# Optimization experiments

Hardware: AMD Instinct MI355X
Metric: run time of the kernel (lower is better)

The kernel has to match this reference:

```python
import jax, jax.numpy as jnp
import numpy as np

N = 50000          # number of nodes
A = 32             # anchor_set_num
D = 64             # latdim


def setup_inputs() -> dict:
    key = jax.random.key(0)
    k1, k2, k3, k4, k5 = jax.random.split(key, 5)
    embeds = jax.random.normal(k1, (N, D), dtype=jnp.float32)
    dists_array = jax.random.uniform(k2, (A, N), dtype=jnp.float32)
    anchor_set_id = jax.random.randint(k3, (A,), 0, N)
    # nn.Linear(2*latdim, latdim): weight [D, 2D], bias [D]
    bound = 1.0 / np.sqrt(2 * D)
    W_hidden = jax.random.uniform(k4, (D, 2 * D), minval=-bound, maxval=bound, dtype=jnp.float32)
    b_hidden = jax.random.uniform(k5, (D,), minval=-bound, maxval=bound, dtype=jnp.float32)
    return {"embeds": embeds, "dists_array": dists_array,
            "anchor_set_id": anchor_set_id,
            "W_hidden": W_hidden, "b_hidden": b_hidden}


def reference(embeds, dists_array, anchor_set_id, W_hidden, b_hidden):
    n, d = embeds.shape
    a = anchor_set_id.shape[0]
    # set_ids_emb.repeat(N,1).reshape(N, A, D) reduces to broadcasting anchors over nodes
    set_ids_emb = embeds[anchor_set_id]                       # [A, D]
    # messages[n, a] = set_ids_emb[a] * dists[a, n]
    messages = set_ids_emb[None, :, :] * dists_array.T[:, :, None]   # [N, A, D]
    # embeds.repeat(A,1).reshape(N, A, D): element [i, j] = embeds[(i*A + j) % N]
    self_feature = jnp.tile(embeds, (a, 1)).reshape(n, a, d)         # [N, A, D]
    # concat + Linear(2D -> D) expressed as split matmul (same math, no concat buffer)
    W1 = W_hidden[:, :d]   # acts on messages
    W2 = W_hidden[:, d:]   # acts on self_feature
    hidden = (jnp.einsum('nad,kd->nak', messages, W1)
              + jnp.einsum('nad,kd->nak', self_feature, W2)
              + b_hidden)                                            # [N, A, D]
    return jnp.mean(hidden, axis=1)                                  # [N, D]
```

## Files before the change

kernel.cpp:

```cpp
#include <hip/hip_runtime.h>


constexpr int N_PTS  = 50000;
constexpr int A_ANCH = 32;
constexpr int D_DIM  = 64;
constexpr int NSB    = 3125;
constexpr int TN     = 16;
constexpr int TILES  = N_PTS / TN;
constexpr int XSTR   = 36;
constexpr int PREP_TILE   = 16;
constexpr int PREP_BLOCKS = (NSB + PREP_TILE - 1) / PREP_TILE;

__global__ __launch_bounds__(256) void prep_kernel(
        const float* __restrict__ embeds,
        const int*   __restrict__ aid,
        const float* __restrict__ W,
        float*       __restrict__ M1,
        float*       __restrict__ SBW)
{
    const int t = threadIdx.x;

    if (blockIdx.x == PREP_BLOCKS) {
        for (int idx = t; idx < A_ANCH * D_DIM; idx += 256) {
            int a = idx >> 6, k = idx & 63;
            const float* erow = embeds + (size_t)aid[a] * D_DIM;
            const float* wrow = W + (size_t)k * 128;
            float s = 0.0f;
#pragma unroll
            for (int d = 0; d < D_DIM; ++d) s += erow[d] * wrow[d];
            M1[idx] = s * (1.0f / 32.0f);
        }
        return;
    }

    __shared__ float w2[64 * 64];
    __shared__ float sb[PREP_TILE * 64];

    {
        int k  = t & 63;
        int d0 = (t >> 6) * 16;
        const float* wr = W + (size_t)k * 128 + 64;
#pragma unroll
        for (int q = 0; q < 16; ++q) w2[(d0 + q) * 64 + k] = wr[d0 + q];
    }

    const int i0 = blockIdx.x * PREP_TILE;
    {
        int d = t & 63, il0 = t >> 6;
        for (int il = il0; il < PREP_TILE; il += 4) {
            int i = i0 + il;
            if (i >= NSB) break;
            int base = 16 * i;
            float s = 0.0f;
#pragma unroll
            for (int j = 0; j < 32; ++j) {
                int r = base + j;
                if (r >= N_PTS) r -= N_PTS;
                s += embeds[(size_t)r * D_DIM + d];
            }
            sb[il * 64 + d] = s;
        }
    }
    __syncthreads();
    {
        int k = t & 63, il0 = t >> 6;
        for (int il = il0; il < PREP_TILE; il += 4) {
            int i = i0 + il;
            if (i >= NSB) break;
            const float* srow = sb + il * 64;
            float s = 0.0f;
#pragma unroll
            for (int d = 0; d < D_DIM; ++d) s += srow[d] * w2[d * 64 + k];
            SBW[(size_t)i * 64 + k] = s * (1.0f / 32.0f);
        }
    }
}

__global__ __launch_bounds__(256, 4) void pnn_main(
        const float* __restrict__ dists,
        const float* __restrict__ b,
        const float* __restrict__ M1,
        const float* __restrict__ SBW,
        float*       __restrict__ out)
{
    __shared__ float m1s[A_ANCH * D_DIM];
    __shared__ float xs[TN * XSTR];

    const int t = threadIdx.x;

    {
        const float4* M4 = (const float4*)M1;
        float4*       s4 = (float4*)m1s;
#pragma unroll
        for (int q = 0; q < 2; ++q) s4[t + 256 * q] = M4[t + 256 * q];
    }

    const int lane_k  = t & 15;
    const int n_local = t >> 4;
    const int k0      = lane_k * 4;
    const float4 bias = *(const float4*)(b + k0);

    for (int tile = blockIdx.x; tile < TILES; tile += gridDim.x) {
        const int n0 = tile * TN;
        const int n  = n0 + n_local;
        const int i  = (2 * n) % NSB;
        float4 sbw = *(const float4*)(SBW + (size_t)i * D_DIM + k0);

        __syncthreads();
        for (int q = t; q < A_ANCH * TN; q += 256) {
            int a  = q >> 4;
            int nl = q & 15;
            xs[nl * XSTR + a] = dists[(size_t)a * N_PTS + n0 + nl];
        }
        __syncthreads();

        float4 acc;
        acc.x = bias.x + sbw.x; acc.y = bias.y + sbw.y;
        acc.z = bias.z + sbw.z; acc.w = bias.w + sbw.w;

        const float* xrow = xs + n_local * XSTR;
#pragma unroll
        for (int jj = 0; jj < A_ANCH; jj += 4) {
            float4 xv = *(const float4*)(xrow + jj);
            float4 w0 = *(const float4*)(m1s + (jj + 0) * 64 + k0);
            float4 w1 = *(const float4*)(m1s + (jj + 1) * 64 + k0);
            float4 w2 = *(const float4*)(m1s + (jj + 2) * 64 + k0);
            float4 w3 = *(const float4*)(m1s + (jj + 3) * 64 + k0);
            acc.x += xv.x * w0.x; acc.y += xv.x * w0.y; acc.z += xv.x * w0.z; acc.w += xv.x * w0.w;
            acc.x += xv.y * w1.x; acc.y += xv.y * w1.y; acc.z += xv.y * w1.z; acc.w += xv.y * w1.w;
            acc.x += xv.z * w2.x; acc.y += xv.z * w2.y; acc.z += xv.z * w2.z; acc.w += xv.z * w2.w;
            acc.x += xv.w * w3.x; acc.y += xv.w * w3.y; acc.z += xv.w * w3.z; acc.w += xv.w * w3.w;
        }
        *(float4*)(out + (size_t)n * D_DIM + k0) = acc;
    }
}

extern "C" void kernel_launch(void* const* d_in, const int* in_sizes, int n_in,
                              void* d_out, int out_size, void* d_ws, size_t ws_size,
                              hipStream_t stream) {
    const float* embeds = (const float*)d_in[0];
    const float* dists  = (const float*)d_in[1];
    const int*   aid    = (const int*)  d_in[2];
    const float* W      = (const float*)d_in[3];
    const float* b      = (const float*)d_in[4];
    float*       out    = (float*)d_out;

    float* M1  = (float*)d_ws;
    float* SBW = (float*)d_ws + A_ANCH * D_DIM;

    prep_kernel<<<PREP_BLOCKS + 1, 256, 0, stream>>>(embeds, aid, W, M1, SBW);
    pnn_main<<<782, 256, 0, stream>>>(dists, b, M1, SBW, out);
}
```

Measured before the change: 102.3 us.

## Double-buffer dists tiles in shared memory with nontemporal loads/stores

Prefetches the next tile's dists slice into a second shared buffer while computing the current tile, replacing two barriers per iteration with one. Uses nontemporal loads for dists and nontemporal stores for the output to reduce cache pollution. Also halves the prep kernel tile size to spread its work across more blocks. Adds shared memory and some register pressure, and each block only has a few iterations to overlap.

```diff
diff --git a/kernel.cpp b/kernel.cpp
--- a/kernel.cpp
+++ b/kernel.cpp
@@ -1,5 +1,7 @@
 #include <hip/hip_runtime.h>
 
+
+typedef float f32x4 __attribute__((ext_vector_type(4)));
 
 constexpr int N_PTS  = 50000;
 constexpr int A_ANCH = 32;
@@ -8,8 +10,9 @@
 constexpr int TN     = 16;
 constexpr int TILES  = N_PTS / TN;
 constexpr int XSTR   = 36;
-constexpr int PREP_TILE   = 16;
+constexpr int PREP_TILE   = 8;
 constexpr int PREP_BLOCKS = (NSB + PREP_TILE - 1) / PREP_TILE;
+constexpr int MAIN_GRID   = 782;
 
 __global__ __launch_bounds__(256) void prep_kernel(
         const float* __restrict__ embeds,
@@ -46,8 +49,8 @@
 
     const int i0 = blockIdx.x * PREP_TILE;
     {
-        int d = t & 63, il0 = t >> 6;
-        for (int il = il0; il < PREP_TILE; il += 4) {
+        int d = t & 63, il = t >> 6;
+        for (; il < PREP_TILE; il += 4) {
             int i = i0 + il;
             if (i >= NSB) break;
             int base = 16 * i;
@@ -63,8 +66,8 @@
     }
     __syncthreads();
     {
-        int k = t & 63, il0 = t >> 6;
-        for (int il = il0; il < PREP_TILE; il += 4) {
+        int k = t & 63, il = t >> 6;
+        for (; il < PREP_TILE; il += 4) {
             int i = i0 + il;
             if (i >= NSB) break;
             const float* srow = sb + il * 64;
@@ -84,7 +87,7 @@
         float*       __restrict__ out)
 {
     __shared__ float m1s[A_ANCH * D_DIM];
-    __shared__ float xs[TN * XSTR];
+    __shared__ float xs[2][TN * XSTR];
 
     const int t = threadIdx.x;
 
@@ -100,25 +103,43 @@
     const int k0      = lane_k * 4;
     const float4 bias = *(const float4*)(b + k0);
 
-    for (int tile = blockIdx.x; tile < TILES; tile += gridDim.x) {
-        const int n0 = tile * TN;
-        const int n  = n0 + n_local;
-        const int i  = (2 * n) % NSB;
+    const int st_a  = t >> 4;
+    const int st_nl = t & 15;
+
+    {
+        const int n0 = blockIdx.x * TN;
+#pragma unroll
+        for (int q = 0; q < 2; ++q) {
+            int a = st_a + 16 * q;
+            xs[0][st_nl * XSTR + a] =
+                __builtin_nontemporal_load(dists + (size_t)a * N_PTS + n0 + st_nl);
+        }
+    }
+    __syncthreads();
+
+    int tile = blockIdx.x;
+    for (int g = 0; tile < TILES; ++g, tile += MAIN_GRID) {
+        const int cur = g & 1;
+        const int n   = tile * TN + n_local;
+        const int i   = (2 * n) % NSB;
         float4 sbw = *(const float4*)(SBW + (size_t)i * D_DIM + k0);
 
-        __syncthreads();
-        for (int q = t; q < A_ANCH * TN; q += 256) {
-            int a  = q >> 4;
-            int nl = q & 15;
-            xs[nl * XSTR + a] = dists[(size_t)a * N_PTS + n0 + nl];
+        const int ntile = tile + MAIN_GRID;
+        if (ntile < TILES) {
+            const int n0 = ntile * TN;
+#pragma unroll
+            for (int q = 0; q < 2; ++q) {
+                int a = st_a + 16 * q;
+                xs[cur ^ 1][st_nl * XSTR + a] =
+                    __builtin_nontemporal_load(dists + (size_t)a * N_PTS + n0 + st_nl);
+            }
         }
-        __syncthreads();
 
         float4 acc;
         acc.x = bias.x + sbw.x; acc.y = bias.y + sbw.y;
         acc.z = bias.z + sbw.z; acc.w = bias.w + sbw.w;
 
-        const float* xrow = xs + n_local * XSTR;
+        const float* xrow = xs[cur] + n_local * XSTR;
 #pragma unroll
         for (int jj = 0; jj < A_ANCH; jj += 4) {
             float4 xv = *(const float4*)(xrow + jj);
@@ -131,7 +152,13 @@
             acc.x += xv.z * w2.x; acc.y += xv.z * w2.y; acc.z += xv.z * w2.z; acc.w += xv.z * w2.w;
             acc.x += xv.w * w3.x; acc.y += xv.w * w3.y; acc.z += xv.w * w3.z; acc.w += xv.w * w3.w;
         }
-        *(float4*)(out + (size_t)n * D_DIM + k0) = acc;
+        {
+            f32x4 accv;
+            accv.x = acc.x; accv.y = acc.y; accv.z = acc.z; accv.w = acc.w;
+            __builtin_nontemporal_store(accv, (f32x4*)(out + (size_t)n * D_DIM + k0));
+        }
+
+        __syncthreads();
     }
 }
 
@@ -149,5 +176,5 @@
     float* SBW = (float*)d_ws + A_ANCH * D_DIM;
 
     prep_kernel<<<PREP_BLOCKS + 1, 256, 0, stream>>>(embeds, aid, W, M1, SBW);
-    pnn_main<<<782, 256, 0, stream>>>(dists, b, M1, SBW, out);
+    pnn_main<<<MAIN_GRID, 256, 0, stream>>>(dists, b, M1, SBW, out);
 }
```

New measurement: 102.4 us. About the same (+0.0%).
